# Kernel optimization log

Hardware: AMD Instinct MI355X
Metric: run time of the kernel (lower is better)

Reference implementation:

```python
import jax, jax.numpy as jnp
import numpy as np

N, E, F_IN, H, D, HID, G = 50000, 800000, 64, 4, 32, 128, 1024
NEG_SLOPE = 0.2


def setup_inputs():
    key = jax.random.key(0)
    ks = jax.random.split(key, 32)
    inp = {
        "x": jax.random.normal(ks[0], (N, F_IN), dtype=jnp.float32),
        "edge_index": jax.random.randint(ks[1], (2, E), 0, N, dtype=jnp.int64),
        "batch": jnp.sort(jax.random.randint(ks[2], (N,), 0, G, dtype=jnp.int64)),
    }
    dims = [F_IN, HID, HID]
    i = 3
    for l, din in enumerate(dims):
        s = 1.0 / np.sqrt(din)
        inp[f"Wl{l}"] = jax.random.normal(ks[i], (din, H * D), dtype=jnp.float32) * s; i += 1
        inp[f"bl{l}"] = jnp.zeros((H * D,), dtype=jnp.float32)
        inp[f"Wr{l}"] = jax.random.normal(ks[i], (din, H * D), dtype=jnp.float32) * s; i += 1
        inp[f"br{l}"] = jnp.zeros((H * D,), dtype=jnp.float32)
        inp[f"att{l}"] = jax.random.normal(ks[i], (H, D), dtype=jnp.float32) * (1.0 / np.sqrt(D)); i += 1
        inp[f"b{l}"] = jnp.zeros((H * D,), dtype=jnp.float32)
    inp["Wh"] = jax.random.normal(ks[i], (HID, 1), dtype=jnp.float32) * (1.0 / np.sqrt(HID))
    inp["bh"] = jnp.zeros((1,), dtype=jnp.float32)
    return inp


def gatv2_layer(x, src, dst, Wl, bl, Wr, br, att, b):
    # GATv2Conv (eval mode, no dropout): e_ij = att . leaky_relu(Wl x_j + Wr x_i)
    xl = (x @ Wl + bl).reshape(-1, H, D)   # source transform
    xr = (x @ Wr + br).reshape(-1, H, D)   # target transform
    m = xl[src] + xr[dst]                  # [E,H,D]
    e = jnp.where(m >= 0, m, NEG_SLOPE * m)
    score = jnp.einsum("ehd,hd->eh", e, att)          # [E,H]
    smax = jax.ops.segment_max(score, dst, num_segments=N)  # [N,H]
    expv = jnp.exp(score - smax[dst])
    denom = jax.ops.segment_sum(expv, dst, num_segments=N)
    alpha = expv / denom[dst]                          # softmax over in-edges of dst
    agg = jax.ops.segment_sum(alpha[:, :, None] * xl[src], dst, num_segments=N)
    return agg.reshape(-1, H * D) + b


def reference(x, edge_index, batch, Wl0, bl0, Wr0, br0, att0, b0,
              Wl1, bl1, Wr1, br1, att1, b1,
              Wl2, bl2, Wr2, br2, att2, b2, Wh, bh):
    src, dst = edge_index[0], edge_index[1]
    params = [(Wl0, bl0, Wr0, br0, att0, b0),
              (Wl1, bl1, Wr1, br1, att1, b1),
              (Wl2, bl2, Wr2, br2, att2, b2)]
    h = x
    for p in params:
        h = gatv2_layer(h, src, dst, *p)
        h = jax.nn.elu(h)  # dropout inactive in eval
    # global mean pool over graphs
    sums = jax.ops.segment_sum(h, batch, num_segments=G)
    cnt = jax.ops.segment_sum(jnp.ones((h.shape[0],), h.dtype), batch, num_segments=G)
    pooled = sums / jnp.maximum(cnt, 1.0)[:, None]
    return pooled @ Wh + bh
```

## Files before the change

kernel.cpp:

```cpp
#include <hip/hip_runtime.h>
#include <math.h>

#define N_NODES 50000
#define N_EDGES 800000
#define HD 128
#define GG 1024
#define NEG_SLOPE 0.2f
#define SCAN_B 1024
#define NB ((N_NODES + SCAN_B - 1) / SCAN_B)
#define NXCONV (N_NODES * 64)

typedef __attribute__((ext_vector_type(8))) short bf16x8;
typedef __attribute__((ext_vector_type(4))) float f32x4;

__device__ __forceinline__ unsigned short f2bf(float v) {
    unsigned u = __float_as_uint(v);
    u += 0x7fff + ((u >> 16) & 1);
    return (unsigned short)(u >> 16);
}
__device__ __forceinline__ float bf2f(unsigned short s) {
    return __uint_as_float((unsigned)s << 16);
}

__global__ void convert_all(const float* __restrict__ x,
                            unsigned short* __restrict__ Xh, unsigned short* __restrict__ Xl,
                            const float* __restrict__ W0l, const float* __restrict__ W0r,
                            const float* __restrict__ W1l, const float* __restrict__ W1r,
                            const float* __restrict__ W2l, const float* __restrict__ W2r,
                            unsigned short* __restrict__ Wth, unsigned short* __restrict__ Wtl,
                            int* __restrict__ deg)
{
    const int i = blockIdx.x * 256 + threadIdx.x;
    if (i < N_NODES) deg[i] = 0;
    if (i < NXCONV) {
        const float v = x[i];
        const unsigned short hi = f2bf(v);
        Xh[i] = hi;
        Xl[i] = f2bf(v - bf2f(hi));
        return;
    }
    const int t = i - NXCONV;
    const float* Wl; const float* Wr;
    int c, k, o;
    if (t < 16384) {
        c = t >> 6; k = t & 63; o = t;
        Wl = W0l; Wr = W0r;
    } else if (t < 49152) {
        const int b = t - 16384; c = b >> 7; k = b & 127; o = 32768 + b;
        Wl = W1l; Wr = W1r;
    } else if (t < 81920) {
        const int b = t - 49152; c = b >> 7; k = b & 127; o = 65536 + b;
        Wl = W2l; Wr = W2r;
    } else return;
    const float v = (c < 128) ? Wl[(size_t)k * 128 + c] : Wr[(size_t)k * 128 + (c - 128)];
    const unsigned short hi = f2bf(v);
    Wth[o] = hi;
    Wtl[o] = f2bf(v - bf2f(hi));
}

__global__ void prep_graph(const int* __restrict__ dst, int* __restrict__ deg,
                           const int* __restrict__ batch, int* __restrict__ gptr)
{
    const int e = blockIdx.x * 256 + threadIdx.x;
    if (e < N_EDGES) atomicAdd(&deg[dst[e]], 1);
    if (e > N_NODES) return;
    if (e == 0) {
        for (int g = 0; g <= batch[0]; g++) gptr[g] = 0;
    } else if (e == N_NODES) {
        for (int g = batch[N_NODES - 1] + 1; g <= GG; g++) gptr[g] = N_NODES;
    } else {
        const int b0 = batch[e - 1], b1 = batch[e];
        for (int g = b0 + 1; g <= b1; g++) gptr[g] = e;
    }
}

template<int K>
__launch_bounds__(256)
__global__ void gemm_reg(const unsigned short* __restrict__ Xh, const unsigned short* __restrict__ Xl,
                         const unsigned short* __restrict__ Wth, const unsigned short* __restrict__ Wtl,
                         const float* __restrict__ bl, const float* __restrict__ br,
                         float* __restrict__ Cl, float* __restrict__ Cr, int n)
{
    constexpr int NCH = K / 32;
    constexpr int RT  = (N_NODES + 63) / 64;
    const int tid  = threadIdx.x;
    const int wave = tid >> 6;
    const int lane = tid & 63;
    const int quad = lane >> 4;
    const int l15  = lane & 15;
    const int wid  = blockIdx.x * 4 + wave;
    const int colid = wid & 7;
    const int cb32  = colid * 32;
    const int rs    = wid >> 3;
    const int NS    = (gridDim.x * 4) >> 3;

    bf16x8 Bh[NCH][2], Bo[NCH][2];
    #pragma unroll
    for (int ch = 0; ch < NCH; ch++)
        #pragma unroll
        for (int nt = 0; nt < 2; nt++) {
            const size_t wo = (size_t)(cb32 + nt * 16 + l15) * K + ch * 32 + quad * 8;
            Bh[ch][nt] = *(const bf16x8*)(Wth + wo);
            Bo[ch][nt] = *(const bf16x8*)(Wtl + wo);
        }

    const int cb = cb32 & 127;
    const float* bias = (colid < 4) ? bl : br;
    float* C = (colid < 4) ? Cl : Cr;
    float bv[2];
    bv[0] = bias[cb + l15];
    bv[1] = bias[cb + 16 + l15];

    for (int rt = rs; rt < RT; rt += NS) {
        const int row0 = rt * 64;
        f32x4 acc[4][2];
        #pragma unroll
        for (int mt = 0; mt < 4; mt++) {
            acc[mt][0] = (f32x4){0.f, 0.f, 0.f, 0.f};
            acc[mt][1] = (f32x4){0.f, 0.f, 0.f, 0.f};
        }
        #pragma unroll
        for (int ch = 0; ch < NCH; ch++) {
            bf16x8 ah[4], al[4];
            #pragma unroll
            for (int mt = 0; mt < 4; mt++) {
                int r = row0 + mt * 16 + l15;
                r = (r < n) ? r : (n - 1);
                const size_t go = (size_t)r * K + ch * 32 + quad * 8;
                ah[mt] = *(const bf16x8*)(Xh + go);
                al[mt] = *(const bf16x8*)(Xl + go);
            }
            #pragma unroll
            for (int nt = 0; nt < 2; nt++)
                #pragma unroll
                for (int mt = 0; mt < 4; mt++) {
                    acc[mt][nt] = __builtin_amdgcn_mfma_f32_16x16x32_bf16(ah[mt], Bh[ch][nt], acc[mt][nt], 0, 0, 0);
                    acc[mt][nt] = __builtin_amdgcn_mfma_f32_16x16x32_bf16(ah[mt], Bo[ch][nt], acc[mt][nt], 0, 0, 0);
                    acc[mt][nt] = __builtin_amdgcn_mfma_f32_16x16x32_bf16(al[mt], Bh[ch][nt], acc[mt][nt], 0, 0, 0);
                }
        }
        #pragma unroll
        for (int nt = 0; nt < 2; nt++)
            #pragma unroll
            for (int mt = 0; mt < 4; mt++)
                #pragma unroll
                for (int r = 0; r < 4; r++) {
                    const int row = row0 + mt * 16 + quad * 4 + r;
                    if (row < n)
                        C[(size_t)row * 128 + cb + nt * 16 + l15] = acc[mt][nt][r] + bv[nt];
                }
    }
}

__launch_bounds__(SCAN_B)
__global__ void scan_block(const int* __restrict__ deg, int* __restrict__ rowptr,
                           int* __restrict__ btot)
{
    __shared__ int s[SCAN_B];
    const int tid = threadIdx.x;
    const int i = blockIdx.x * SCAN_B + tid;
    int v = (i < N_NODES) ? deg[i] : 0;
    s[tid] = v;
    __syncthreads();
    for (int off = 1; off < SCAN_B; off <<= 1) {
        int t = (tid >= off) ? s[tid - off] : 0;
        __syncthreads();
        s[tid] += t;
        __syncthreads();
    }
    if (i < N_NODES) rowptr[i] = s[tid] - v;
    if (tid == SCAN_B - 1) btot[blockIdx.x] = s[SCAN_B - 1];
}

__launch_bounds__(256)
__global__ void scan_add(const int* __restrict__ btot, int* __restrict__ rowptr,
                         int* __restrict__ cursor)
{
    __shared__ int sb[NB + 1];
    const int tid = threadIdx.x;
    if (tid < 64) {
        const int v = (tid < NB) ? btot[tid] : 0;
        int incl = v;
        #pragma unroll
        for (int off = 1; off < 64; off <<= 1) {
            const int t = __shfl_up(incl, off);
            if (tid >= off) incl += t;
        }
        if (tid < NB) sb[tid] = incl - v;
        if (tid == NB - 1) sb[NB] = incl;
    }
    __syncthreads();
    const int i = blockIdx.x * 256 + tid;
    if (i < N_NODES) {
        const int r = rowptr[i] + sb[i >> 10];
        rowptr[i] = r;
        cursor[i] = r;
    }
    if (i == N_NODES) rowptr[N_NODES] = sb[NB];
}

__global__ void scatter_csr(const int* __restrict__ src, const int* __restrict__ dst,
                            int* __restrict__ cursor, int* __restrict__ csr_src)
{
    int e = blockIdx.x * 256 + threadIdx.x;
    if (e >= N_EDGES) return;
    int pos = atomicAdd(&cursor[dst[e]], 1);
    csr_src[pos] = src[e];
}

template<int LAST>
__launch_bounds__(256)
__global__ void node_attn(const float* __restrict__ xl, const float* __restrict__ xr,
                          const int* __restrict__ rowptr, const int* __restrict__ csr_src,
                          const float* __restrict__ att, const float* __restrict__ bvec,
                          unsigned short* __restrict__ Hh, unsigned short* __restrict__ Hl,
                          const float* __restrict__ Wh, float* __restrict__ pernode)
{
    const int node = (blockIdx.x * 256 + threadIdx.x) >> 6;
    const int lane = threadIdx.x & 63;
    if (node >= N_NODES) return;
    const int grp = lane >> 4;
    const int li  = lane & 15;

    const size_t nb = (size_t)node * HD + li * 8;
    const float4 xr0 = *(const float4*)(xr + nb);
    const float4 xr1 = *(const float4*)(xr + nb + 4);
    const float4 aw0 = *(const float4*)(att + li * 8);
    const float4 aw1 = *(const float4*)(att + li * 8 + 4);
    const int beg = rowptr[node];
    const int end = rowptr[node + 1];

    float m = -1e30f, l = 0.f;
    float4 a0 = make_float4(0.f, 0.f, 0.f, 0.f);
    float4 a1 = make_float4(0.f, 0.f, 0.f, 0.f);

    int e0 = beg + grp;
    int s0 = (e0 < end) ? csr_src[e0] : 0;
    float4 v0 = *(const float4*)(xl + (size_t)s0 * HD + li * 8);
    float4 v1 = *(const float4*)(xl + (size_t)s0 * HD + li * 8 + 4);

    for (int base = beg; base < end; base += 4) {
        const bool valid = (base + grp) < end;
        float4 n0 = v0, n1 = v1;
        if (base + 4 < end) {
            const int e2 = base + 4 + grp;
            const int s2 = (e2 < end) ? csr_src[e2] : 0;
            n0 = *(const float4*)(xl + (size_t)s2 * HD + li * 8);
            n1 = *(const float4*)(xl + (size_t)s2 * HD + li * 8 + 4);
        }
        float t, pa, pb;
        t = v0.x + xr0.x; t = fmaxf(t, NEG_SLOPE * t); pa = t * aw0.x;
        t = v0.y + xr0.y; t = fmaxf(t, NEG_SLOPE * t); pb = t * aw0.y;
        t = v0.z + xr0.z; t = fmaxf(t, NEG_SLOPE * t); pa = fmaf(t, aw0.z, pa);
        t = v0.w + xr0.w; t = fmaxf(t, NEG_SLOPE * t); pb = fmaf(t, aw0.w, pb);
        t = v1.x + xr1.x; t = fmaxf(t, NEG_SLOPE * t); pa = fmaf(t, aw1.x, pa);
        t = v1.y + xr1.y; t = fmaxf(t, NEG_SLOPE * t); pb = fmaf(t, aw1.y, pb);
        t = v1.z + xr1.z; t = fmaxf(t, NEG_SLOPE * t); pa = fmaf(t, aw1.z, pa);
        t = v1.w + xr1.w; t = fmaxf(t, NEG_SLOPE * t); pb = fmaf(t, aw1.w, pb);
        float p = pa + pb;
        p += __shfl_xor(p, 1);
        p += __shfl_xor(p, 2);

        const float mn = valid ? fmaxf(m, p) : m;
        const float w  = valid ? __expf(p - mn) : 0.f;
        const float sc = __expf(m - mn);
        l = fmaf(l, sc, w);
        a0.x = fmaf(a0.x, sc, w * v0.x);
        a0.y = fmaf(a0.y, sc, w * v0.y);
        a0.z = fmaf(a0.z, sc, w * v0.z);
        a0.w = fmaf(a0.w, sc, w * v0.w);
        a1.x = fmaf(a1.x, sc, w * v1.x);
        a1.y = fmaf(a1.y, sc, w * v1.y);
        a1.z = fmaf(a1.z, sc, w * v1.z);
        a1.w = fmaf(a1.w, sc, w * v1.w);
        m = mn;
        v0 = n0; v1 = n1;
    }

    #pragma unroll
    for (int off = 16; off < 64; off <<= 1) {
        const float mo = __shfl_xor(m, off);
        const float lo = __shfl_xor(l, off);
        float4 b0, b1;
        b0.x = __shfl_xor(a0.x, off); b0.y = __shfl_xor(a0.y, off);
        b0.z = __shfl_xor(a0.z, off); b0.w = __shfl_xor(a0.w, off);
        b1.x = __shfl_xor(a1.x, off); b1.y = __shfl_xor(a1.y, off);
        b1.z = __shfl_xor(a1.z, off); b1.w = __shfl_xor(a1.w, off);
        const float mm = fmaxf(m, mo);
        const float e1 = __expf(m - mm);
        const float e2 = __expf(mo - mm);
        l = l * e1 + lo * e2;
        a0.x = a0.x * e1 + b0.x * e2;
        a0.y = a0.y * e1 + b0.y * e2;
        a0.z = a0.z * e1 + b0.z * e2;
        a0.w = a0.w * e1 + b0.w * e2;
        a1.x = a1.x * e1 + b1.x * e2;
        a1.y = a1.y * e1 + b1.y * e2;
        a1.z = a1.z * e1 + b1.z * e2;
        a1.w = a1.w * e1 + b1.w * e2;
        m = mm;
    }

    if (grp == 0) {
        const float inv = (l > 0.f) ? 1.f / l : 0.f;
        const float4 bb0 = *(const float4*)(bvec + li * 8);
        const float4 bb1 = *(const float4*)(bvec + li * 8 + 4);
        float o[8];
        o[0] = fmaf(a0.x, inv, bb0.x);
        o[1] = fmaf(a0.y, inv, bb0.y);
        o[2] = fmaf(a0.z, inv, bb0.z);
        o[3] = fmaf(a0.w, inv, bb0.w);
        o[4] = fmaf(a1.x, inv, bb1.x);
        o[5] = fmaf(a1.y, inv, bb1.y);
        o[6] = fmaf(a1.z, inv, bb1.z);
        o[7] = fmaf(a1.w, inv, bb1.w);
        #pragma unroll
        for (int j = 0; j < 8; j++)
            o[j] = (o[j] > 0.f) ? o[j] : expm1f(o[j]);
        if (LAST) {
            const float4 w0 = *(const float4*)(Wh + li * 8);
            const float4 w1 = *(const float4*)(Wh + li * 8 + 4);
            float da = o[0] * w0.x + o[2] * w0.z;
            float db = o[1] * w0.y + o[3] * w0.w;
            da = fmaf(o[4], w1.x, da); db = fmaf(o[5], w1.y, db);
            da = fmaf(o[6], w1.z, da); db = fmaf(o[7], w1.w, db);
            float d = da + db;
            d += __shfl_xor(d, 1);
            d += __shfl_xor(d, 2);
            d += __shfl_xor(d, 4);
            d += __shfl_xor(d, 8);
            if (li == 0) pernode[node] = d;
        } else {
            bf16x8 hv, lv;
            #pragma unroll
            for (int j = 0; j < 8; j++) {
                unsigned short h = f2bf(o[j]);
                hv[j] = (short)h;
                lv[j] = (short)f2bf(o[j] - bf2f(h));
            }
            *(bf16x8*)(Hh + nb) = hv;
            *(bf16x8*)(Hl + nb) = lv;
        }
    }
}

__launch_bounds__(256)
__global__ void finish_head(const float* __restrict__ pernode, const int* __restrict__ gptr,
                            const float* __restrict__ bh, float* __restrict__ out)
{
    const int g = (blockIdx.x * 256 + threadIdx.x) >> 6;
    const int lane = threadIdx.x & 63;
    if (g >= GG) return;
    const int b0 = gptr[g], b1 = gptr[g + 1];
    float s = 0.f;
    for (int i = b0 + lane; i < b1; i += 64) s += pernode[i];
    s += __shfl_xor(s, 1);
    s += __shfl_xor(s, 2);
    s += __shfl_xor(s, 4);
    s += __shfl_xor(s, 8);
    s += __shfl_xor(s, 16);
    s += __shfl_xor(s, 32);
    if (lane == 0) out[g] = s / fmaxf((float)(b1 - b0), 1.f) + bh[0];
}

extern "C" void kernel_launch(void* const* d_in, const int* in_sizes, int n_in,
                              void* d_out, int out_size, void* d_ws, size_t ws_size,
                              hipStream_t stream)
{
    const float* x     = (const float*)d_in[0];
    const int*   edge  = (const int*)d_in[1];
    const int*   batch = (const int*)d_in[2];
    const int*   src   = edge;
    const int*   dst   = edge + N_EDGES;
    const float* Wh    = (const float*)d_in[21];
    const float* bh    = (const float*)d_in[22];
    float* out = (float*)d_out;

    const size_t N128 = (size_t)N_NODES * HD;
    float* buf_xl = (float*)d_ws;
    float* buf_xr = buf_xl + N128;
    unsigned short* Xh  = (unsigned short*)(buf_xr + N128);
    unsigned short* Xl_ = Xh + N128;
    unsigned short* Wth = Xl_ + N128;
    unsigned short* Wtl = Wth + 3 * 256 * 128;
    int* deg       = (int*)(Wtl + 3 * 256 * 128);
    float* pernode = (float*)(deg + N_NODES);
    int* rowptr  = (int*)(pernode + N_NODES);
    int* cursor  = rowptr + N_NODES + 1;
    int* csr_src = cursor + N_NODES;
    int* btot    = csr_src + N_EDGES;
    int* gptr    = btot + NB;

    convert_all<<<(NXCONV + 81920 + 255) / 256, 256, 0, stream>>>(
        x, Xh, Xl_,
        (const float*)d_in[3], (const float*)d_in[5],
        (const float*)d_in[9], (const float*)d_in[11],
        (const float*)d_in[15], (const float*)d_in[17],
        Wth, Wtl, deg);
    prep_graph<<<(N_EDGES + 255) / 256, 256, 0, stream>>>(dst, deg, batch, gptr);
    scan_block<<<NB, SCAN_B, 0, stream>>>(deg, rowptr, btot);
    scan_add<<<(N_NODES + 256) / 256, 256, 0, stream>>>(btot, rowptr, cursor);
    scatter_csr<<<(N_EDGES + 255) / 256, 256, 0, stream>>>(src, dst, cursor, csr_src);

    const int gemm_grid = 768;
    const int attn_grid = (N_NODES + 3) / 4;

    for (int l = 0; l < 3; l++) {
        const float* bl  = (const float*)d_in[4 + 6 * l];
        const float* br  = (const float*)d_in[6 + 6 * l];
        const float* att = (const float*)d_in[7 + 6 * l];
        const float* bb  = (const float*)d_in[8 + 6 * l];

        if (l == 0)
            gemm_reg<64><<<gemm_grid, 256, 0, stream>>>(Xh, Xl_, Wth, Wtl,
                                                        bl, br, buf_xl, buf_xr, N_NODES);
        else
            gemm_reg<128><<<gemm_grid, 256, 0, stream>>>(Xh, Xl_,
                                                         Wth + l * 256 * 128, Wtl + l * 256 * 128,
                                                         bl, br, buf_xl, buf_xr, N_NODES);
        if (l < 2)
            node_attn<0><<<attn_grid, 256, 0, stream>>>(buf_xl, buf_xr, rowptr, csr_src,
                                                        att, bb, Xh, Xl_,
                                                        nullptr, nullptr);
        else
            node_attn<1><<<attn_grid, 256, 0, stream>>>(buf_xl, buf_xr, rowptr, csr_src,
                                                        att, bb, nullptr, nullptr,
                                                        Wh, pernode);
    }

    finish_head<<<GG / 4, 256, 0, stream>>>(pernode, gptr, bh, out);
}
```

Measured before the change: 486.3 us.

## Stage input row tiles in LDS and launch one block per row tile

The node-feature GEMM now loads each 64-row slab of the bf16 hi/lo inputs into padded shared memory once per block. Each block's four waves then read their fragments from shared memory instead of each wave reloading them from global memory. The persistent grid-stride loop is replaced by one block per (row tile, column half), launched with a min-blocks-per-SM hint. The aim is to cut redundant global reads of X, at the cost of reloading the weight fragments into registers in every block and adding a shared-memory barrier.

```diff
diff --git a/kernel.cpp b/kernel.cpp
--- a/kernel.cpp
+++ b/kernel.cpp
@@ -75,24 +75,25 @@
 }
 
 template<int K>
-__launch_bounds__(256)
-__global__ void gemm_reg(const unsigned short* __restrict__ Xh, const unsigned short* __restrict__ Xl,
+__launch_bounds__(256, 3)
+__global__ void gemm_lds(const unsigned short* __restrict__ Xh, const unsigned short* __restrict__ Xl,
                          const unsigned short* __restrict__ Wth, const unsigned short* __restrict__ Wtl,
                          const float* __restrict__ bl, const float* __restrict__ br,
                          float* __restrict__ Cl, float* __restrict__ Cr, int n)
 {
     constexpr int NCH = K / 32;
-    constexpr int RT  = (N_NODES + 63) / 64;
+    constexpr int STR = K + 8;
+    __shared__ unsigned short AsH[64 * STR], AsL[64 * STR];
     const int tid  = threadIdx.x;
     const int wave = tid >> 6;
     const int lane = tid & 63;
     const int quad = lane >> 4;
     const int l15  = lane & 15;
-    const int wid  = blockIdx.x * 4 + wave;
-    const int colid = wid & 7;
+    const int cg   = blockIdx.x & 1;
+    const int rt   = blockIdx.x >> 1;
+    const int row0 = rt * 64;
+    const int colid = cg * 4 + wave;
     const int cb32  = colid * 32;
-    const int rs    = wid >> 3;
-    const int NS    = (gridDim.x * 4) >> 3;
 
     bf16x8 Bh[NCH][2], Bo[NCH][2];
     #pragma unroll
@@ -104,51 +105,62 @@
             Bo[ch][nt] = *(const bf16x8*)(Wtl + wo);
         }
 
+    {
+        constexpr int THR = K / 8;
+        constexpr int RPP = 256 / THR;
+        const int sr = tid / THR, seg = tid % THR;
+        #pragma unroll
+        for (int ps = 0; ps < 64 / RPP; ps++) {
+            const int r = ps * RPP + sr;
+            int gr = row0 + r;
+            gr = (gr < n) ? gr : (n - 1);
+            const size_t go = (size_t)gr * K + seg * 8;
+            *(uint4*)&AsH[r * STR + seg * 8] = *(const uint4*)(Xh + go);
+            *(uint4*)&AsL[r * STR + seg * 8] = *(const uint4*)(Xl + go);
+        }
+    }
+    __syncthreads();
+
+    f32x4 acc[4][2];
+    #pragma unroll
+    for (int mt = 0; mt < 4; mt++) {
+        acc[mt][0] = (f32x4){0.f, 0.f, 0.f, 0.f};
+        acc[mt][1] = (f32x4){0.f, 0.f, 0.f, 0.f};
+    }
+    #pragma unroll
+    for (int ch = 0; ch < NCH; ch++) {
+        bf16x8 ah[4], al[4];
+        #pragma unroll
+        for (int mt = 0; mt < 4; mt++) {
+            ah[mt] = *(const bf16x8*)&AsH[(mt * 16 + l15) * STR + ch * 32 + quad * 8];
+            al[mt] = *(const bf16x8*)&AsL[(mt * 16 + l15) * STR + ch * 32 + quad * 8];
+        }
+        #pragma unroll
+        for (int nt = 0; nt < 2; nt++)
+            #pragma unroll
+            for (int mt = 0; mt < 4; mt++) {
+                acc[mt][nt] = __builtin_amdgcn_mfma_f32_16x16x32_bf16(ah[mt], Bh[ch][nt], acc[mt][nt], 0, 0, 0);
+                acc[mt][nt] = __builtin_amdgcn_mfma_f32_16x16x32_bf16(ah[mt], Bo[ch][nt], acc[mt][nt], 0, 0, 0);
+                acc[mt][nt] = __builtin_amdgcn_mfma_f32_16x16x32_bf16(al[mt], Bh[ch][nt], acc[mt][nt], 0, 0, 0);
+            }
+    }
+
     const int cb = cb32 & 127;
     const float* bias = (colid < 4) ? bl : br;
     float* C = (colid < 4) ? Cl : Cr;
-    float bv[2];
-    bv[0] = bias[cb + l15];
-    bv[1] = bias[cb + 16 + l15];
-
-    for (int rt = rs; rt < RT; rt += NS) {
-        const int row0 = rt * 64;
-        f32x4 acc[4][2];
-        #pragma unroll
-        for (int mt = 0; mt < 4; mt++) {
-            acc[mt][0] = (f32x4){0.f, 0.f, 0.f, 0.f};
-            acc[mt][1] = (f32x4){0.f, 0.f, 0.f, 0.f};
-        }
-        #pragma unroll
-        for (int ch = 0; ch < NCH; ch++) {
-            bf16x8 ah[4], al[4];
+    const float bv0 = bias[cb + l15];
+    const float bv1 = bias[cb + 16 + l15];
+    #pragma unroll
+    for (int nt = 0; nt < 2; nt++) {
+        const float bv = nt ? bv1 : bv0;
+        #pragma unroll
+        for (int mt = 0; mt < 4; mt++)
             #pragma unroll
-            for (int mt = 0; mt < 4; mt++) {
-                int r = row0 + mt * 16 + l15;
-                r = (r < n) ? r : (n - 1);
-                const size_t go = (size_t)r * K + ch * 32 + quad * 8;
-                ah[mt] = *(const bf16x8*)(Xh + go);
-                al[mt] = *(const bf16x8*)(Xl + go);
+            for (int r = 0; r < 4; r++) {
+                const int row = row0 + mt * 16 + quad * 4 + r;
+                if (row < n)
+                    C[(size_t)row * 128 + cb + nt * 16 + l15] = acc[mt][nt][r] + bv;
             }
-            #pragma unroll
-            for (int nt = 0; nt < 2; nt++)
-                #pragma unroll
-                for (int mt = 0; mt < 4; mt++) {
-                    acc[mt][nt] = __builtin_amdgcn_mfma_f32_16x16x32_bf16(ah[mt], Bh[ch][nt], acc[mt][nt], 0, 0, 0);
-                    acc[mt][nt] = __builtin_amdgcn_mfma_f32_16x16x32_bf16(ah[mt], Bo[ch][nt], acc[mt][nt], 0, 0, 0);
-                    acc[mt][nt] = __builtin_amdgcn_mfma_f32_16x16x32_bf16(al[mt], Bh[ch][nt], acc[mt][nt], 0, 0, 0);
-                }
-        }
-        #pragma unroll
-        for (int nt = 0; nt < 2; nt++)
-            #pragma unroll
-            for (int mt = 0; mt < 4; mt++)
-                #pragma unroll
-                for (int r = 0; r < 4; r++) {
-                    const int row = row0 + mt * 16 + quad * 4 + r;
-                    if (row < n)
-                        C[(size_t)row * 128 + cb + nt * 16 + l15] = acc[mt][nt][r] + bv[nt];
-                }
     }
 }
 
@@ -402,7 +414,7 @@
     scan_add<<<(N_NODES + 256) / 256, 256, 0, stream>>>(btot, rowptr, cursor);
     scatter_csr<<<(N_EDGES + 255) / 256, 256, 0, stream>>>(src, dst, cursor, csr_src);
 
-    const int gemm_grid = 768;
+    const int gemm_grid = ((N_NODES + 63) / 64) * 2;
     const int attn_grid = (N_NODES + 3) / 4;
 
     for (int l = 0; l < 3; l++) {
@@ -412,10 +424,10 @@
         const float* bb  = (const float*)d_in[8 + 6 * l];
 
         if (l == 0)
-            gemm_reg<64><<<gemm_grid, 256, 0, stream>>>(Xh, Xl_, Wth, Wtl,
+            gemm_lds<64><<<gemm_grid, 256, 0, stream>>>(Xh, Xl_, Wth, Wtl,
                                                         bl, br, buf_xl, buf_xr, N_NODES);
         else
-            gemm_reg<128><<<gemm_grid, 256, 0, stream>>>(Xh, Xl_,
+            gemm_lds<128><<<gemm_grid, 256, 0, stream>>>(Xh, Xl_,
                                                          Wth + l * 256 * 128, Wtl + l * 256 * 128,
                                                          bl, br, buf_xl, buf_xr, N_NODES);
         if (l < 2)
```

New measurement: 478.5 us. About the same (-1.6%).
